# Optimization experiments

Hardware: AMD Instinct MI355X
Metric: run time of the kernel (lower is better)

Reference implementation:

```python
import jax, jax.numpy as jnp
import numpy as np


def setup_inputs() -> dict:
    key = jax.random.key(0)
    k1, k2 = jax.random.split(key)
    x = jax.random.normal(k1, (8, 128, 128, 128), dtype=jnp.float32)        # [N, C, H, W]
    codebook = jax.random.normal(k2, (256, 128), dtype=jnp.float32)         # [K, C] class_emb_vecs
    return {"x": x, "codebook": codebook}


def reference(x, codebook):
    # Brute-force 1-NN with p=2 (Euclidean), matching sklearn NearestNeighbors(brute, p=2).
    # argmin ||q - c||_2 == argmin (||q||^2 - 2 q.c + ||c||^2), so use the GEMM form.
    N, C, H, W = x.shape
    q = jnp.transpose(x, (0, 2, 3, 1)).reshape(-1, C)       # [N*H*W, C], matches x.reshape(-1, C) channel-last? 
    # NOTE: torch x.reshape(-1, C) on [N,C,H,W] flattens with C as the fastest-varying of the
    # leading dims only when memory layout is NCHW -> rows are (n, c_blocks)... Torch's
    # reshape(-1, C) actually slices contiguous groups of C elements along W. To be faithful
    # to x.reshape(-1, C) on a contiguous NCHW tensor:
    q = x.reshape(-1, C)                                     # [N*C*H*W/C, C] — same elements, same order as torch
    q_sq = jnp.sum(q * q, axis=1, keepdims=True)             # [M, 1]
    c_sq = jnp.sum(codebook * codebook, axis=1)              # [K]
    # squared distances: [M, K]
    d2 = q_sq - 2.0 * (q @ codebook.T) + c_sq[None, :]
    idx = jnp.argmin(d2, axis=1).astype(jnp.int32)           # [M]
    return idx.reshape(N, H, W)
```

## Files before the change

kernel.cpp:

```cpp
#include <hip/hip_runtime.h>
#include <hip/hip_bf16.h>


typedef __bf16 bf16x8 __attribute__((ext_vector_type(8)));
typedef float  floatx4 __attribute__((ext_vector_type(4)));

#define MFMA16 __builtin_amdgcn_mfma_f32_16x16x32_bf16

#define CNT_OFF 0
#define CSQ_OFF 1024
#define CBB_OFF 4096
#define WL_OFF  (4096 + 131072)
#define WL_CAP  32768
#define T_FLAG  0.004f

__device__ __forceinline__ unsigned fmap(float f) {
    unsigned u = __float_as_uint(f);
    return (u & 0x80000000u) ? ~u : (u | 0x80000000u);
}
__device__ __forceinline__ float unfmap(unsigned u) {
    unsigned b = (u & 0x80000000u) ? (u ^ 0x80000000u) : ~u;
    return __uint_as_float(b);
}

__global__ void knn_prep(const float* __restrict__ cb, __bf16* __restrict__ cbB,
                         float* __restrict__ csq, int* __restrict__ cnt) {
    const int tid = threadIdx.x;
    const int id = blockIdx.x * 256 + tid;
    if (id == 0) *cnt = 0;
    const int part = id >> 12;
    const int rem = id & 4095;
    const int t4 = rem >> 8;
    const int kb = (rem >> 6) & 3;
    const int ln = id & 63;
    const int n = t4 * 16 + (ln & 15);
    const int k0 = kb * 32 + (ln >> 4) * 8;
    const float* src = cb + (size_t)n * 128 + k0;
    union { __bf16 h[8]; uint4 u; } p;
#pragma unroll
    for (int j = 0; j < 8; ++j) {
        float f = src[j];
        __bf16 hh = (__bf16)f;
        p.h[j] = (part == 0) ? hh : (__bf16)(f - (float)hh);
    }
    *(uint4*)(cbB + (size_t)id * 8) = p.u;

    if (blockIdx.x == 0) {
        const float4* row = (const float4*)(cb + (size_t)tid * 128);
        float a0 = 0.f, a1 = 0.f, a2 = 0.f, a3 = 0.f;
#pragma unroll 8
        for (int j = 0; j < 32; ++j) {
            float4 v = row[j];
            a0 = fmaf(v.x, v.x, a0);
            a1 = fmaf(v.y, v.y, a1);
            a2 = fmaf(v.z, v.z, a2);
            a3 = fmaf(v.w, v.w, a3);
        }
        csq[tid] = (a0 + a1) + (a2 + a3);
    }
}

__global__ __launch_bounds__(256, 2) void knn_mfma(const float* __restrict__ x,
                                                   const __bf16* __restrict__ cbB,
                                                   const float* __restrict__ csq_g,
                                                   int* __restrict__ out,
                                                   int* __restrict__ cnt,
                                                   int* __restrict__ wl) {
    __shared__ __bf16 sB[32768];
    __shared__ float s_csq[256];

    const int tid = threadIdx.x;
    const int wave = tid >> 6;
    const int lane = tid & 63;
    const int rl = lane & 15;
    const int kg = lane >> 4;

    s_csq[tid] = csq_g[tid];

    const float* xq = x + ((size_t)blockIdx.x * 128 + wave * 32) * 128;
    bf16x8 ah[2][4], al[2][4];
#pragma unroll
    for (int m = 0; m < 2; ++m) {
#pragma unroll
        for (int kb = 0; kb < 4; ++kb) {
            const float* s = xq + (size_t)(m * 16 + rl) * 128 + kb * 32 + kg * 8;
            float4 f0 = *(const float4*)(s);
            float4 f1 = *(const float4*)(s + 4);
            float f[8] = {f0.x, f0.y, f0.z, f0.w, f1.x, f1.y, f1.z, f1.w};
            union { __bf16 h[8]; bf16x8 v; } ph, pl;
#pragma unroll
            for (int j = 0; j < 8; ++j) {
                __bf16 hh = (__bf16)f[j];
                ph.h[j] = hh;
                pl.h[j] = (__bf16)(f[j] - (float)hh);
            }
            ah[m][kb] = ph.v;
            al[m][kb] = pl.v;
        }
    }

    {
        const uint4* src = (const uint4*)cbB;
        uint4* dst = (uint4*)sB;
#pragma unroll 4
        for (int i = 0; i < 16; ++i) dst[i * 256 + tid] = src[i * 256 + tid];
    }
    __syncthreads();

    floatx4 acc[2][16];
#pragma unroll
    for (int m = 0; m < 2; ++m)
#pragma unroll
        for (int t = 0; t < 16; ++t) acc[m][t] = (floatx4){0.f, 0.f, 0.f, 0.f};

#pragma unroll
    for (int kb = 0; kb < 4; ++kb) {
#pragma unroll
        for (int t = 0; t < 16; ++t) {
            bf16x8 b = *(const bf16x8*)(sB + (((t * 4 + kb) * 64 + lane) * 8));
            acc[0][t] = MFMA16(ah[0][kb], b, acc[0][t], 0, 0, 0);
            acc[1][t] = MFMA16(ah[1][kb], b, acc[1][t], 0, 0, 0);
            acc[0][t] = MFMA16(al[0][kb], b, acc[0][t], 0, 0, 0);
            acc[1][t] = MFMA16(al[1][kb], b, acc[1][t], 0, 0, 0);
        }
    }
    __syncthreads();

    {
        const uint4* src = (const uint4*)(cbB + 32768);
        uint4* dst = (uint4*)sB;
#pragma unroll 4
        for (int i = 0; i < 16; ++i) dst[i * 256 + tid] = src[i * 256 + tid];
    }
    __syncthreads();

#pragma unroll
    for (int kb = 0; kb < 4; ++kb) {
#pragma unroll
        for (int t = 0; t < 16; ++t) {
            bf16x8 b = *(const bf16x8*)(sB + (((t * 4 + kb) * 64 + lane) * 8));
            acc[0][t] = MFMA16(ah[0][kb], b, acc[0][t], 0, 0, 0);
            acc[1][t] = MFMA16(ah[1][kb], b, acc[1][t], 0, 0, 0);
        }
    }

    float cs[16];
#pragma unroll
    for (int t = 0; t < 16; ++t) cs[t] = s_csq[t * 16 + rl];

#pragma unroll
    for (int m = 0; m < 2; ++m) {
#pragma unroll
        for (int r = 0; r < 4; ++r) {
            unsigned long long b = ~0ULL, s = ~0ULL;
#pragma unroll
            for (int t = 0; t < 16; ++t) {
                const int n = t * 16 + rl;
                float score = fmaf(-2.0f, acc[m][t][r], cs[t]);
                unsigned long long key =
                    ((unsigned long long)fmap(score) << 32) | (unsigned)n;
                if (key < b) { s = b; b = key; }
                else if (key < s) { s = key; }
            }
#pragma unroll
            for (int d = 1; d < 16; d <<= 1) {
                unsigned long long ob = __shfl_xor(b, d);
                unsigned long long os = __shfl_xor(s, d);
                unsigned long long nb = ob < b ? ob : b;
                unsigned long long mx = ob < b ? b : ob;
                unsigned long long mn = os < s ? os : s;
                b = nb;
                s = mx < mn ? mx : mn;
            }
            if (rl == 0) {
                const size_t qg = (size_t)blockIdx.x * 128 + wave * 32
                                  + m * 16 + kg * 4 + r;
                out[qg] = (int)(unsigned)(b & 0xFFFFFFFFull);
                float f1 = unfmap((unsigned)(b >> 32));
                float f2 = unfmap((unsigned)(s >> 32));
                if (f2 - f1 < T_FLAG) {
                    int idx = atomicAdd(cnt, 1);
                    if (idx < WL_CAP) wl[idx] = (int)qg;
                }
            }
        }
    }
}

__global__ __launch_bounds__(256) void knn_refine(const float* __restrict__ x,
                                                  const float* __restrict__ cb,
                                                  const float* __restrict__ csq_g,
                                                  const int* __restrict__ wl,
                                                  const int* __restrict__ cnt,
                                                  int* __restrict__ out) {
    __shared__ unsigned long long sP[4];
    const int tid = threadIdx.x;
    const int lane = tid & 63;
    const int wave = tid >> 6;

    int n = *cnt;
    if (n > WL_CAP) n = WL_CAP;
    const float mycsq = csq_g[tid];
    const float4* cr = (const float4*)(cb + (size_t)tid * 128);

    for (int i = blockIdx.x; i < n; i += gridDim.x) {
        const int q = wl[i];
        const float4* qr = (const float4*)(x + (size_t)q * 128);
        float a0 = 0.f, a1 = 0.f, a2 = 0.f, a3 = 0.f;
#pragma unroll 8
        for (int c4 = 0; c4 < 32; ++c4) {
            float4 qv = qr[c4];
            float4 cv = cr[c4];
            a0 = fmaf(qv.x, cv.x, a0);
            a1 = fmaf(qv.y, cv.y, a1);
            a2 = fmaf(qv.z, cv.z, a2);
            a3 = fmaf(qv.w, cv.w, a3);
        }
        float dot = (a0 + a1) + (a2 + a3);
        float score = fmaf(-2.0f, dot, mycsq);
        unsigned long long key =
            ((unsigned long long)fmap(score) << 32) | (unsigned)tid;
#pragma unroll
        for (int d = 1; d < 64; d <<= 1) {
            unsigned long long o = __shfl_xor(key, d);
            key = o < key ? o : key;
        }
        if (lane == 0) sP[wave] = key;
        __syncthreads();
        if (tid == 0) {
            unsigned long long b = sP[0];
            unsigned long long o;
            o = sP[1]; b = o < b ? o : b;
            o = sP[2]; b = o < b ? o : b;
            o = sP[3]; b = o < b ? o : b;
            out[q] = (int)(unsigned)(b & 0xFFFFFFFFull);
        }
        __syncthreads();
    }
}

extern "C" void kernel_launch(void* const* d_in, const int* in_sizes, int n_in,
                              void* d_out, int out_size, void* d_ws, size_t ws_size,
                              hipStream_t stream) {
    const float* x = (const float*)d_in[0];
    const float* cb = (const float*)d_in[1];
    int* out = (int*)d_out;

    char* ws = (char*)d_ws;
    int* cnt = (int*)(ws + CNT_OFF);
    float* csq = (float*)(ws + CSQ_OFF);
    __bf16* cbB = (__bf16*)(ws + CBB_OFF);
    int* wl = (int*)(ws + WL_OFF);

    const int M = in_sizes[0] / 128;

    knn_prep<<<32, 256, 0, stream>>>(cb, cbB, csq, cnt);
    knn_mfma<<<M / 128, 256, 0, stream>>>(x, cbB, csq, out, cnt, wl);
    knn_refine<<<240, 256, 0, stream>>>(x, cb, csq, wl, cnt, out);
}
```

Measured before the change: 134.9 us.

## Split codebook across wave pairs and halve queries per block

Each block now handles 64 queries instead of 128. The four waves form a 2x2 grid: each wave covers 32 queries against half of the codebook, and the two halves' best and second-best keys are merged through shared memory. This doubles the grid size and halves the accumulator registers per wave, which is meant to improve occupancy and load balance. In exchange, each block still copies the full 64KB bf16 codebook into LDS, so codebook staging traffic per query doubles, and an extra barrier plus a merge step are added.

Result: slower. 145.3 us (+7.7%).

```diff
diff --git a/kernel.cpp b/kernel.cpp
--- a/kernel.cpp
+++ b/kernel.cpp
@@ -68,16 +68,20 @@
                                                    int* __restrict__ wl) {
     __shared__ __bf16 sB[32768];
     __shared__ float s_csq[256];
+    __shared__ unsigned long long sWb[128];
+    __shared__ unsigned long long sWs[128];
 
     const int tid = threadIdx.x;
     const int wave = tid >> 6;
     const int lane = tid & 63;
+    const int mg = wave >> 1;
+    const int ng = wave & 1;
     const int rl = lane & 15;
     const int kg = lane >> 4;
 
     s_csq[tid] = csq_g[tid];
 
-    const float* xq = x + ((size_t)blockIdx.x * 128 + wave * 32) * 128;
+    const float* xq = x + ((size_t)blockIdx.x * 64 + mg * 32) * 128;
     bf16x8 ah[2][4], al[2][4];
 #pragma unroll
     for (int m = 0; m < 2; ++m) {
@@ -107,17 +111,18 @@
     }
     __syncthreads();
 
-    floatx4 acc[2][16];
+    floatx4 acc[2][8];
 #pragma unroll
     for (int m = 0; m < 2; ++m)
 #pragma unroll
-        for (int t = 0; t < 16; ++t) acc[m][t] = (floatx4){0.f, 0.f, 0.f, 0.f};
+        for (int t = 0; t < 8; ++t) acc[m][t] = (floatx4){0.f, 0.f, 0.f, 0.f};
 
 #pragma unroll
     for (int kb = 0; kb < 4; ++kb) {
 #pragma unroll
-        for (int t = 0; t < 16; ++t) {
-            bf16x8 b = *(const bf16x8*)(sB + (((t * 4 + kb) * 64 + lane) * 8));
+        for (int t = 0; t < 8; ++t) {
+            const int t4 = ng * 8 + t;
+            bf16x8 b = *(const bf16x8*)(sB + (((t4 * 4 + kb) * 64 + lane) * 8));
             acc[0][t] = MFMA16(ah[0][kb], b, acc[0][t], 0, 0, 0);
             acc[1][t] = MFMA16(ah[1][kb], b, acc[1][t], 0, 0, 0);
             acc[0][t] = MFMA16(al[0][kb], b, acc[0][t], 0, 0, 0);
@@ -137,16 +142,17 @@
 #pragma unroll
     for (int kb = 0; kb < 4; ++kb) {
 #pragma unroll
-        for (int t = 0; t < 16; ++t) {
-            bf16x8 b = *(const bf16x8*)(sB + (((t * 4 + kb) * 64 + lane) * 8));
+        for (int t = 0; t < 8; ++t) {
+            const int t4 = ng * 8 + t;
+            bf16x8 b = *(const bf16x8*)(sB + (((t4 * 4 + kb) * 64 + lane) * 8));
             acc[0][t] = MFMA16(ah[0][kb], b, acc[0][t], 0, 0, 0);
             acc[1][t] = MFMA16(ah[1][kb], b, acc[1][t], 0, 0, 0);
         }
     }
 
-    float cs[16];
-#pragma unroll
-    for (int t = 0; t < 16; ++t) cs[t] = s_csq[t * 16 + rl];
+    float cs[8];
+#pragma unroll
+    for (int t = 0; t < 8; ++t) cs[t] = s_csq[(ng * 8 + t) * 16 + rl];
 
 #pragma unroll
     for (int m = 0; m < 2; ++m) {
@@ -154,8 +160,8 @@
         for (int r = 0; r < 4; ++r) {
             unsigned long long b = ~0ULL, s = ~0ULL;
 #pragma unroll
-            for (int t = 0; t < 16; ++t) {
-                const int n = t * 16 + rl;
+            for (int t = 0; t < 8; ++t) {
+                const int n = (ng * 8 + t) * 16 + rl;
                 float score = fmaf(-2.0f, acc[m][t][r], cs[t]);
                 unsigned long long key =
                     ((unsigned long long)fmap(score) << 32) | (unsigned)n;
@@ -173,16 +179,28 @@
                 s = mx < mn ? mx : mn;
             }
             if (rl == 0) {
-                const size_t qg = (size_t)blockIdx.x * 128 + wave * 32
-                                  + m * 16 + kg * 4 + r;
-                out[qg] = (int)(unsigned)(b & 0xFFFFFFFFull);
-                float f1 = unfmap((unsigned)(b >> 32));
-                float f2 = unfmap((unsigned)(s >> 32));
-                if (f2 - f1 < T_FLAG) {
-                    int idx = atomicAdd(cnt, 1);
-                    if (idx < WL_CAP) wl[idx] = (int)qg;
-                }
-            }
+                const int ql = mg * 32 + m * 16 + kg * 4 + r;
+                sWb[ql * 2 + ng] = b;
+                sWs[ql * 2 + ng] = s;
+            }
+        }
+    }
+    __syncthreads();
+
+    if (tid < 64) {
+        unsigned long long b0 = sWb[tid * 2 + 0], b1 = sWb[tid * 2 + 1];
+        unsigned long long s0 = sWs[tid * 2 + 0], s1 = sWs[tid * 2 + 1];
+        unsigned long long best = b0 < b1 ? b0 : b1;
+        unsigned long long mx = b0 < b1 ? b1 : b0;
+        unsigned long long mn = s0 < s1 ? s0 : s1;
+        unsigned long long sec = mx < mn ? mx : mn;
+        const size_t qg = (size_t)blockIdx.x * 64 + tid;
+        out[qg] = (int)(unsigned)(best & 0xFFFFFFFFull);
+        float f1 = unfmap((unsigned)(best >> 32));
+        float f2 = unfmap((unsigned)(sec >> 32));
+        if (f2 - f1 < T_FLAG) {
+            int idx = atomicAdd(cnt, 1);
+            if (idx < WL_CAP) wl[idx] = (int)qg;
         }
     }
 }
@@ -255,6 +273,6 @@
     const int M = in_sizes[0] / 128;
 
     knn_prep<<<32, 256, 0, stream>>>(cb, cbB, csq, cnt);
-    knn_mfma<<<M / 128, 256, 0, stream>>>(x, cbB, csq, out, cnt, wl);
+    knn_mfma<<<M / 64, 256, 0, stream>>>(x, cbB, csq, out, cnt, wl);
     knn_refine<<<240, 256, 0, stream>>>(x, cb, csq, wl, cnt, out);
 }
```
